# Performance work log

Measured on AMD Instinct MI355X. Metric: run time of the kernel, lower is better.

## Reference

```python
import jax, jax.numpy as jnp
import numpy as np

B, S, E, H, Dh = 2, 2048, 1024, 16, 64


def setup_inputs() -> dict:
    key = jax.random.key(0)
    ks = jax.random.split(key, 12)
    scale = 1.0 / np.sqrt(E)
    inp = {
        "query": jax.random.normal(ks[0], (B, S, E), jnp.float32),
        "key_": jax.random.normal(ks[1], (B, S, E), jnp.float32),
        "value": jax.random.normal(ks[2], (B, S, E), jnp.float32),
        # causal mask, broadcast over heads inside reference (mask==0 -> -inf)
        "mask": jnp.broadcast_to(jnp.tril(jnp.ones((S, S), jnp.int32)), (B, S, S)),
        "WQ": jax.random.normal(ks[3], (E, H * Dh), jnp.float32) * scale,
        "bQ": jnp.zeros((H * Dh,), jnp.float32),
        "WK": jax.random.normal(ks[4], (E, H * Dh), jnp.float32) * scale,
        "bK": jnp.zeros((H * Dh,), jnp.float32),
        "WV": jax.random.normal(ks[5], (E, H * Dh), jnp.float32) * scale,
        "bV": jnp.zeros((H * Dh,), jnp.float32),
        "WO": jax.random.normal(ks[6], (H * Dh, E), jnp.float32) * scale,
        "bO": jnp.zeros((E,), jnp.float32),
    }
    return inp


def reference(query, key_, value, mask, WQ, bQ, WK, bK, WV, bV, WO, bO):
    # projections -> [B, H, S, Dh]
    def proj(x, W, b):
        y = x @ W + b  # [B, S, H*Dh]
        return y.reshape(B, -1, H, Dh).transpose(0, 2, 1, 3)

    q = proj(query, WQ, bQ)
    k = proj(key_, WK, bK)
    v = proj(value, WV, bV)

    # scores [B, H, S, S]
    a = jnp.einsum("bhqd,bhkd->bhqk", q, k) / jnp.sqrt(jnp.float32(Dh))
    a = jnp.where(mask[:, None, :, :] == 0, -jnp.inf, a)
    alpha = jax.nn.softmax(a, axis=-1)
    z = jnp.einsum("bhqk,bhkd->bhqd", alpha, v)  # [B, H, S, Dh]
    z = z.transpose(0, 2, 1, 3).reshape(B, -1, H * Dh)
    return z @ WO + bO
```

## Files before the change

### kernel.cpp

```cpp
#include <hip/hip_runtime.h>
#include <hip/hip_bf16.h>
#include <math.h>

namespace {

constexpr int Bb = 2, Ss = 2048, Ee = 1024, Hh = 16, Dh = 64;
constexpr int M  = Bb * Ss;
constexpr int N  = Hh * Dh;
constexpr int Kd = Ee;

typedef __attribute__((ext_vector_type(8))) short bf16x8;
typedef __attribute__((ext_vector_type(4))) float f32x4;

__device__ inline float bflo(unsigned u) { return __uint_as_float(u << 16); }
__device__ inline float bfhi(unsigned u) { return __uint_as_float(u & 0xffff0000u); }
__device__ inline unsigned short f2bf(float f) {
  return __builtin_bit_cast(unsigned short, __float2bfloat16(f));
}
__device__ inline unsigned pack2(float a, float b) {
  return (unsigned)f2bf(a) | ((unsigned)f2bf(b) << 16);
}
__device__ inline void load_lds16(const void* g, void* lds) {
  __builtin_amdgcn_global_load_lds((const __attribute__((address_space(1))) void*)g,
                                   (__attribute__((address_space(3))) void*)lds, 16, 0, 0);
}

__global__ __launch_bounds__(256) void convert3(const float* __restrict__ a0,
                                                const float* __restrict__ a1,
                                                const float* __restrict__ a2,
                                                unsigned short* __restrict__ o0,
                                                unsigned short* __restrict__ o1,
                                                unsigned short* __restrict__ o2) {
  const float* src = blockIdx.z == 0 ? a0 : (blockIdx.z == 1 ? a1 : a2);
  unsigned short* dst = blockIdx.z == 0 ? o0 : (blockIdx.z == 1 ? o1 : o2);
  size_t i = ((size_t)blockIdx.x * 256 + threadIdx.x) * 8;
  float4 u = ((const float4*)(src + i))[0];
  float4 v = ((const float4*)(src + i))[1];
  uint4 w;
  w.x = pack2(u.x, u.y);
  w.y = pack2(u.z, u.w);
  w.z = pack2(v.x, v.y);
  w.w = pack2(v.z, v.w);
  *((uint4*)(dst + i)) = w;
}

__global__ __launch_bounds__(256) void transposeW(const float* __restrict__ w0,
                                                  const float* __restrict__ w1,
                                                  const float* __restrict__ w2,
                                                  const float* __restrict__ w3,
                                                  unsigned short* __restrict__ t0,
                                                  unsigned short* __restrict__ t1,
                                                  unsigned short* __restrict__ t2,
                                                  unsigned short* __restrict__ t3) {
  const float* W = blockIdx.z == 0 ? w0 : (blockIdx.z == 1 ? w1 : (blockIdx.z == 2 ? w2 : w3));
  unsigned short* Wt = blockIdx.z == 0 ? t0 : (blockIdx.z == 1 ? t1 : (blockIdx.z == 2 ? t2 : t3));
  __shared__ float tl[32][33];
  const int t = threadIdx.x;
  const int r = t >> 5, c = t & 31;
  const int n0 = blockIdx.x * 32, k0 = blockIdx.y * 32;
#pragma unroll
  for (int i = 0; i < 4; ++i) tl[r + i * 8][c] = W[(size_t)(k0 + r + i * 8) * N + n0 + c];
  __syncthreads();
#pragma unroll
  for (int i = 0; i < 4; ++i) {
    int rr = r + i * 8;
    Wt[(size_t)(n0 + rr) * Kd + k0 + c] = f2bf(tl[c][rr]);
  }
}

template <int PERM>
__global__ __launch_bounds__(256) void gemm_mfma(const unsigned short* __restrict__ A,
                                                 const unsigned short* __restrict__ Wt,
                                                 const float* __restrict__ bias,
                                                 void* __restrict__ Cout, float oscale) {
  __shared__ alignas(16) unsigned short As[128 * 32];
  __shared__ alignas(16) unsigned short Bs[128 * 32];

  const int t  = threadIdx.x;
  const int l  = t & 63;
  const int w  = t >> 6;
  const int wr = w >> 1, wc = w & 1;
  const int lr = l & 15, kc = l >> 4;
  const int bm = blockIdx.y * 128, bn = blockIdx.x * 128;

  f32x4 acc[4][4] = {};

  const int srow = t >> 2, sc = t & 3;
  unsigned short* aD1 = As + (size_t)(w * 64) * 8;
  unsigned short* aD2 = As + (size_t)(w * 64 + 256) * 8;
  unsigned short* bD1 = Bs + (size_t)(w * 64) * 8;
  unsigned short* bD2 = Bs + (size_t)(w * 64 + 256) * 8;
  const unsigned short* Ap1 = A  + (size_t)(bm + srow) * Kd + sc * 8;
  const unsigned short* Ap2 = A  + (size_t)(bm + srow + 64) * Kd + sc * 8;
  const unsigned short* Bp1 = Wt + (size_t)(bn + srow) * Kd + sc * 8;
  const unsigned short* Bp2 = Wt + (size_t)(bn + srow + 64) * Kd + sc * 8;

  for (int kk = 0; kk < Kd; kk += 32) {
    load_lds16(Ap1 + kk, aD1);
    load_lds16(Ap2 + kk, aD2);
    load_lds16(Bp1 + kk, bD1);
    load_lds16(Bp2 + kk, bD2);
    __syncthreads();

    bf16x8 a[4], b[4];
#pragma unroll
    for (int m = 0; m < 4; ++m)
      a[m] = *(const bf16x8*)&As[(size_t)(wr * 64 + m * 16 + lr) * 32 + kc * 8];
#pragma unroll
    for (int n = 0; n < 4; ++n)
      b[n] = *(const bf16x8*)&Bs[(size_t)(wc * 64 + n * 16 + lr) * 32 + kc * 8];
#pragma unroll
    for (int m = 0; m < 4; ++m)
#pragma unroll
      for (int n = 0; n < 4; ++n)
        acc[m][n] = __builtin_amdgcn_mfma_f32_16x16x32_bf16(a[m], b[n], acc[m][n], 0, 0, 0);
    __syncthreads();
  }

#pragma unroll
  for (int m = 0; m < 4; ++m) {
#pragma unroll
    for (int n = 0; n < 4; ++n) {
      const int cg = bn + wc * 64 + n * 16 + lr;
      const float bv = bias[cg];
      f32x4 v = acc[m][n];
      if (PERM == 2) {
        const int rg0 = bm + wr * 64 + m * 16 + kc * 4;
        const int b_ = rg0 >> 11, s0 = rg0 & (Ss - 1);
        const int h = cg >> 6, d = cg & (Dh - 1);
        ushort4 pk;
        pk.x = f2bf((v[0] + bv) * oscale);
        pk.y = f2bf((v[1] + bv) * oscale);
        pk.z = f2bf((v[2] + bv) * oscale);
        pk.w = f2bf((v[3] + bv) * oscale);
        *(ushort4*)((unsigned short*)Cout +
                    (((size_t)(b_ * Hh + h) * Dh + d) << 11) + s0) = pk;
      } else {
#pragma unroll
        for (int r = 0; r < 4; ++r) {
          const int rg  = bm + wr * 64 + m * 16 + kc * 4 + r;
          const float x = (v[r] + bv) * oscale;
          if (PERM == 0) {
            ((float*)Cout)[(size_t)rg * N + cg] = x;
          } else {
            const int b_ = rg >> 11, s = rg & (Ss - 1);
            const int h  = cg >> 6, d = cg & (Dh - 1);
            ((unsigned short*)Cout)[(((size_t)(b_ * Hh + h) * Ss + s) << 6) + d] = f2bf(x);
          }
        }
      }
    }
  }
}

__global__ __launch_bounds__(256) void attn_mfma(const unsigned short* __restrict__ Q,
                                                 const unsigned short* __restrict__ K,
                                                 const unsigned short* __restrict__ Vt,
                                                 unsigned short* __restrict__ Z) {
  __shared__ alignas(16) unsigned short Ks[64 * 64];
  __shared__ alignas(16) unsigned short Vs[64 * 64];
  __shared__ alignas(16) unsigned short Ps[4][16 * 64];

  const int bh = blockIdx.x;
  const int qt = blockIdx.y;
  const int b  = bh >> 4, h = bh & 15;
  const int t  = threadIdx.x;
  const int l  = t & 63;
  const int w  = t >> 6;
  const int lr = l & 15;
  const int lg = l >> 4;

  const int qrow = qt * 64 + w * 16 + lr;
  const unsigned short* Qp = Q + ((size_t)bh * Ss + qrow) * Dh;
  bf16x8 bq[2];
  bq[0] = *(const bf16x8*)(Qp + lg * 8);
  bq[1] = *(const bf16x8*)(Qp + 32 + lg * 8);

  f32x4 o[4] = {};
  float mrow = -INFINITY, lsum = 0.f;

  const int srow = l >> 3;
  const int scol = ((l & 7) ^ srow) * 16;
  const char* Kg = (const char*)(K + (size_t)bh * Ss * Dh);
  const char* Vg = (const char*)(Vt + (size_t)bh * Dh * Ss);
  unsigned short* kD0 = Ks + (w * 16) * 64;
  unsigned short* kD1 = Ks + (w * 16 + 8) * 64;
  unsigned short* vD0 = Vs + (w * 16) * 64;
  unsigned short* vD1 = Vs + (w * 16 + 8) * 64;
  const char* vr0 = Vg + (size_t)(w * 16 + srow) * (Ss * 2) + scol;
  const char* vr1 = Vg + (size_t)(w * 16 + 8 + srow) * (Ss * 2) + scol;

  const int rx = (lr & 7) << 4;

  const int kv_tiles = qt + 1;
  for (int kt = 0; kt < kv_tiles; ++kt) {
    const int kv0 = kt * 64;
    __syncthreads();
    load_lds16(Kg + (size_t)(kv0 + w * 16 + srow) * 128 + scol, kD0);
    load_lds16(Kg + (size_t)(kv0 + w * 16 + 8 + srow) * 128 + scol, kD1);
    load_lds16(vr0 + kv0 * 2, vD0);
    load_lds16(vr1 + kv0 * 2, vD1);
    __syncthreads();

    f32x4 sa[4];
#pragma unroll
    for (int f = 0; f < 4; ++f) {
      sa[f] = (f32x4){0.f, 0.f, 0.f, 0.f};
#pragma unroll
      for (int kk = 0; kk < 2; ++kk) {
        const int cb = (kk * 64 + lg * 16) ^ rx;
        bf16x8 ak = *(const bf16x8*)((const char*)Ks + (f * 16 + lr) * 128 + cb);
        sa[f] = __builtin_amdgcn_mfma_f32_16x16x32_bf16(ak, bq[kk], sa[f], 0, 0, 0);
      }
    }

    if (kt == kv_tiles - 1) {
#pragma unroll
      for (int f = 0; f < 4; ++f)
#pragma unroll
        for (int r = 0; r < 4; ++r) {
          const int kg = kv0 + f * 16 + lg * 4 + r;
          if (kg > qrow) sa[f][r] = -INFINITY;
        }
    }

    float pmax = sa[0][0];
#pragma unroll
    for (int f = 0; f < 4; ++f)
#pragma unroll
      for (int r = 0; r < 4; ++r) pmax = fmaxf(pmax, sa[f][r]);
    pmax = fmaxf(pmax, __shfl_xor(pmax, 16));
    pmax = fmaxf(pmax, __shfl_xor(pmax, 32));
    const float mnew = fmaxf(mrow, pmax);
    const float sc   = __expf(mrow - mnew);

    float p[4][4];
    float psum = 0.f;
#pragma unroll
    for (int f = 0; f < 4; ++f)
#pragma unroll
      for (int r = 0; r < 4; ++r) {
        p[f][r] = __expf(sa[f][r] - mnew);
        psum += p[f][r];
      }
    psum += __shfl_xor(psum, 16);
    psum += __shfl_xor(psum, 32);
    lsum = lsum * sc + psum;
    mrow = mnew;

    float scr[4];
#pragma unroll
    for (int r = 0; r < 4; ++r) scr[r] = __shfl(sc, lg * 4 + r);
#pragma unroll
    for (int n = 0; n < 4; ++n)
#pragma unroll
      for (int r = 0; r < 4; ++r) o[n][r] *= scr[r];

    {
      char* Pw = (char*)Ps[w] + lr * 128;
#pragma unroll
      for (int f = 0; f < 4; ++f) {
        const int k0b = f * 32 + lg * 8;
        *(unsigned*)(Pw + ((k0b) ^ rx))     = pack2(p[f][0], p[f][1]);
        *(unsigned*)(Pw + ((k0b + 4) ^ rx)) = pack2(p[f][2], p[f][3]);
      }
    }

#pragma unroll
    for (int kk = 0; kk < 2; ++kk) {
      const int cb = (kk * 64 + lg * 16) ^ rx;
      bf16x8 ap = *(const bf16x8*)((const char*)Ps[w] + lr * 128 + cb);
#pragma unroll
      for (int n = 0; n < 4; ++n) {
        bf16x8 bv = *(const bf16x8*)((const char*)Vs + (n * 16 + lr) * 128 + cb);
        o[n] = __builtin_amdgcn_mfma_f32_16x16x32_bf16(ap, bv, o[n], 0, 0, 0);
      }
    }
  }

  const float linv = 1.f / lsum;
  float li[4];
#pragma unroll
  for (int r = 0; r < 4; ++r) li[r] = __shfl(linv, lg * 4 + r);
#pragma unroll
  for (int n = 0; n < 4; ++n)
#pragma unroll
    for (int r = 0; r < 4; ++r) {
      const int qg = qt * 64 + w * 16 + lg * 4 + r;
      Z[((size_t)(b * Ss + qg)) * N + h * 64 + n * 16 + lr] =
          f2bf(o[n][r] * li[r]);
    }
}

}

extern "C" void kernel_launch(void* const* d_in, const int* in_sizes, int n_in,
                              void* d_out, int out_size, void* d_ws, size_t ws_size,
                              hipStream_t stream) {
  const float* query = (const float*)d_in[0];
  const float* key_  = (const float*)d_in[1];
  const float* value = (const float*)d_in[2];
  const float* WQ = (const float*)d_in[4];
  const float* bQ = (const float*)d_in[5];
  const float* WK = (const float*)d_in[6];
  const float* bK = (const float*)d_in[7];
  const float* WV = (const float*)d_in[8];
  const float* bV = (const float*)d_in[9];
  const float* WO = (const float*)d_in[10];
  const float* bO = (const float*)d_in[11];
  float* out = (float*)d_out;

  const size_t mat = (size_t)M * N;
  unsigned short* qb  = (unsigned short*)d_ws;
  unsigned short* kb  = qb + mat;
  unsigned short* vb  = kb + mat;
  unsigned short* wqT = vb + mat;
  unsigned short* wkT = wqT + (size_t)N * Kd;
  unsigned short* wvT = wkT + (size_t)N * Kd;
  unsigned short* woT = wvT + (size_t)N * Kd;
  unsigned short* Qw  = woT + (size_t)N * Kd;
  unsigned short* Kw  = Qw + mat;
  unsigned short* Vw  = Kw + mat;
  unsigned short* zb  = qb;

  convert3<<<dim3(mat / (256 * 8), 1, 3), 256, 0, stream>>>(query, key_, value, qb, kb, vb);
  transposeW<<<dim3(N / 32, Kd / 32, 4), 256, 0, stream>>>(WQ, WK, WV, WO, wqT, wkT, wvT, woT);

  dim3 gGemm(N / 128, M / 128);
  gemm_mfma<1><<<gGemm, 256, 0, stream>>>(qb, wqT, bQ, Qw, 0.125f);
  gemm_mfma<1><<<gGemm, 256, 0, stream>>>(kb, wkT, bK, Kw, 1.0f);
  gemm_mfma<2><<<gGemm, 256, 0, stream>>>(vb, wvT, bV, Vw, 1.0f);

  dim3 gAttn(Bb * Hh, Ss / 64);
  attn_mfma<<<gAttn, 256, 0, stream>>>(Qw, Kw, Vw, zb);

  gemm_mfma<0><<<gGemm, 256, 0, stream>>>(zb, woT, bO, out, 1.0f);
}
```

Measured before the change: 300.6 us.

## Double-buffer GEMM LDS tiles, batch QKV projections, stage V transpose via LDS

The GEMM main loop now uses two LDS buffers, so the async global-to-LDS load of the next K-slice is issued while MFMAs run on the current one. The three Q/K/V projection launches are merged into one grid with a z dimension, which cuts launch overhead and fills the GPU with more blocks. The transposed V output is first staged through LDS and then written with coalesced 16-byte stores instead of scattered 8-byte ones. The cost is twice the LDS per block, which may lower occupancy, plus extra barriers in the V epilogue.

```diff
diff --git a/kernel.cpp b/kernel.cpp
--- a/kernel.cpp
+++ b/kernel.cpp
@@ -12,8 +12,6 @@
 typedef __attribute__((ext_vector_type(8))) short bf16x8;
 typedef __attribute__((ext_vector_type(4))) float f32x4;
 
-__device__ inline float bflo(unsigned u) { return __uint_as_float(u << 16); }
-__device__ inline float bfhi(unsigned u) { return __uint_as_float(u & 0xffff0000u); }
 __device__ inline unsigned short f2bf(float f) {
   return __builtin_bit_cast(unsigned short, __float2bfloat16(f));
 }
@@ -68,89 +66,151 @@
   }
 }
 
-template <int PERM>
-__global__ __launch_bounds__(256) void gemm_mfma(const unsigned short* __restrict__ A,
-                                                 const unsigned short* __restrict__ Wt,
-                                                 const float* __restrict__ bias,
-                                                 void* __restrict__ Cout, float oscale) {
-  __shared__ alignas(16) unsigned short As[128 * 32];
-  __shared__ alignas(16) unsigned short Bs[128 * 32];
-
-  const int t  = threadIdx.x;
-  const int l  = t & 63;
-  const int w  = t >> 6;
-  const int wr = w >> 1, wc = w & 1;
-  const int lr = l & 15, kc = l >> 4;
+__device__ __attribute__((always_inline)) inline void gemm_core(
+    const unsigned short* __restrict__ A, const unsigned short* __restrict__ Wt,
+    unsigned short* As0, unsigned short* As1, unsigned short* Bs0,
+    unsigned short* Bs1, f32x4 (&acc)[4][4]) {
+  const int t = threadIdx.x, l = t & 63, w = t >> 6;
+  const int wr = w >> 1, wc = w & 1, lr = l & 15, kc = l >> 4;
   const int bm = blockIdx.y * 128, bn = blockIdx.x * 128;
-
-  f32x4 acc[4][4] = {};
-
-  const int srow = t >> 2, sc = t & 3;
-  unsigned short* aD1 = As + (size_t)(w * 64) * 8;
-  unsigned short* aD2 = As + (size_t)(w * 64 + 256) * 8;
-  unsigned short* bD1 = Bs + (size_t)(w * 64) * 8;
-  unsigned short* bD2 = Bs + (size_t)(w * 64 + 256) * 8;
-  const unsigned short* Ap1 = A  + (size_t)(bm + srow) * Kd + sc * 8;
-  const unsigned short* Ap2 = A  + (size_t)(bm + srow + 64) * Kd + sc * 8;
-  const unsigned short* Bp1 = Wt + (size_t)(bn + srow) * Kd + sc * 8;
-  const unsigned short* Bp2 = Wt + (size_t)(bn + srow + 64) * Kd + sc * 8;
-
-  for (int kk = 0; kk < Kd; kk += 32) {
-    load_lds16(Ap1 + kk, aD1);
-    load_lds16(Ap2 + kk, aD2);
-    load_lds16(Bp1 + kk, bD1);
-    load_lds16(Bp2 + kk, bD2);
-    __syncthreads();
-
+  const int srow = t >> 2, sc4 = t & 3;
+  const unsigned short* Ap1 = A + (size_t)(bm + srow) * Kd + sc4 * 8;
+  const unsigned short* Ap2 = Ap1 + (size_t)64 * Kd;
+  const unsigned short* Bp1 = Wt + (size_t)(bn + srow) * Kd + sc4 * 8;
+  const unsigned short* Bp2 = Bp1 + (size_t)64 * Kd;
+  const size_t d1 = (size_t)(w * 64) * 8, d2 = (size_t)(w * 64 + 256) * 8;
+
+  auto stage = [&](unsigned short* Ab, unsigned short* Bb, int kk) {
+    load_lds16(Ap1 + kk, Ab + d1);
+    load_lds16(Ap2 + kk, Ab + d2);
+    load_lds16(Bp1 + kk, Bb + d1);
+    load_lds16(Bp2 + kk, Bb + d2);
+  };
+  auto compute = [&](const unsigned short* Ab, const unsigned short* Bb) {
     bf16x8 a[4], b[4];
 #pragma unroll
     for (int m = 0; m < 4; ++m)
-      a[m] = *(const bf16x8*)&As[(size_t)(wr * 64 + m * 16 + lr) * 32 + kc * 8];
+      a[m] = *(const bf16x8*)&Ab[(size_t)(wr * 64 + m * 16 + lr) * 32 + kc * 8];
 #pragma unroll
     for (int n = 0; n < 4; ++n)
-      b[n] = *(const bf16x8*)&Bs[(size_t)(wc * 64 + n * 16 + lr) * 32 + kc * 8];
+      b[n] = *(const bf16x8*)&Bb[(size_t)(wc * 64 + n * 16 + lr) * 32 + kc * 8];
 #pragma unroll
     for (int m = 0; m < 4; ++m)
 #pragma unroll
       for (int n = 0; n < 4; ++n)
         acc[m][n] = __builtin_amdgcn_mfma_f32_16x16x32_bf16(a[m], b[n], acc[m][n], 0, 0, 0);
+  };
+
+  stage(As0, Bs0, 0);
+  __syncthreads();
+  for (int kk = 0; kk < Kd; kk += 64) {
+    if (kk + 32 < Kd) stage(As1, Bs1, kk + 32);
+    compute(As0, Bs0);
+    __syncthreads();
+    if (kk + 64 < Kd) stage(As0, Bs0, kk + 64);
+    compute(As1, Bs1);
     __syncthreads();
   }
-
-#pragma unroll
-  for (int m = 0; m < 4; ++m) {
+}
+
+__global__ __launch_bounds__(256) void qkv_gemm(
+    const unsigned short* __restrict__ qb, const unsigned short* __restrict__ kb,
+    const unsigned short* __restrict__ vb, const unsigned short* __restrict__ wqT,
+    const unsigned short* __restrict__ wkT, const unsigned short* __restrict__ wvT,
+    const float* __restrict__ bQ, const float* __restrict__ bK,
+    const float* __restrict__ bV, unsigned short* __restrict__ Qw,
+    unsigned short* __restrict__ Kw, unsigned short* __restrict__ Vt) {
+  __shared__ alignas(16) unsigned short smem[4][128 * 32];
+  const int z = blockIdx.z;
+  const unsigned short* A  = z == 0 ? qb : (z == 1 ? kb : vb);
+  const unsigned short* Wt = z == 0 ? wqT : (z == 1 ? wkT : wvT);
+  const float* bias        = z == 0 ? bQ : (z == 1 ? bK : bV);
+
+  f32x4 acc[4][4] = {};
+  gemm_core(A, Wt, smem[0], smem[1], smem[2], smem[3], acc);
+
+  const int t = threadIdx.x, l = t & 63, w = t >> 6;
+  const int wr = w >> 1, wc = w & 1, lr = l & 15, kc = l >> 4;
+  const int bm = blockIdx.y * 128, bn = blockIdx.x * 128;
+
+  if (z <= 1) {
+    unsigned short* Cout = z ? Kw : Qw;
+    const float oscale = z ? 1.0f : 0.125f;
+#pragma unroll
+    for (int m = 0; m < 4; ++m)
+#pragma unroll
+      for (int n = 0; n < 4; ++n) {
+        const int cg = bn + wc * 64 + n * 16 + lr;
+        const float bv = bias[cg];
+#pragma unroll
+        for (int r = 0; r < 4; ++r) {
+          const int rg = bm + wr * 64 + m * 16 + kc * 4 + r;
+          const int b_ = rg >> 11, s = rg & (Ss - 1);
+          const int h = cg >> 6, d = cg & 63;
+          Cout[(((size_t)(b_ * Hh + h) * Ss + s) << 6) + d] =
+              f2bf((acc[m][n][r] + bv) * oscale);
+        }
+      }
+  } else {
+    unsigned short(*Ct)[136] = reinterpret_cast<unsigned short(*)[136]>(&smem[0][0]);
+    const int b_ = bm >> 11, sb = bm & (Ss - 1);
+#pragma unroll
+    for (int nh = 0; nh < 2; ++nh) {
+      if (wc == nh) {
+#pragma unroll
+        for (int m = 0; m < 4; ++m)
+#pragma unroll
+          for (int n = 0; n < 4; ++n) {
+            const int cg = bn + wc * 64 + n * 16 + lr;
+            const float bv = bias[cg];
+            const int cl = n * 16 + lr;
+            const int s0 = wr * 64 + m * 16 + kc * 4;
+            ushort4 pk;
+            pk.x = f2bf(acc[m][n][0] + bv);
+            pk.y = f2bf(acc[m][n][1] + bv);
+            pk.z = f2bf(acc[m][n][2] + bv);
+            pk.w = f2bf(acc[m][n][3] + bv);
+            *(ushort4*)&Ct[cl][s0] = pk;
+          }
+      }
+      __syncthreads();
+#pragma unroll
+      for (int i = 0; i < 4; ++i) {
+        const int c = i * 256 + t;
+        const int cl = c >> 4, ch = c & 15;
+        const int cg = bn + nh * 64 + cl;
+        const int h = cg >> 6, d = cg & 63;
+        uint4 vv = *(const uint4*)&Ct[cl][ch * 8];
+        *(uint4*)(Vt + (((size_t)(b_ * Hh + h) * Dh + d) << 11) + sb + ch * 8) = vv;
+      }
+      __syncthreads();
+    }
+  }
+}
+
+__global__ __launch_bounds__(256) void gemm_out(const unsigned short* __restrict__ A,
+                                                const unsigned short* __restrict__ Wt,
+                                                const float* __restrict__ bias,
+                                                float* __restrict__ C) {
+  __shared__ alignas(16) unsigned short smem[4][128 * 32];
+  f32x4 acc[4][4] = {};
+  gemm_core(A, Wt, smem[0], smem[1], smem[2], smem[3], acc);
+
+  const int t = threadIdx.x, l = t & 63, w = t >> 6;
+  const int wr = w >> 1, wc = w & 1, lr = l & 15, kc = l >> 4;
+  const int bm = blockIdx.y * 128, bn = blockIdx.x * 128;
+#pragma unroll
+  for (int m = 0; m < 4; ++m)
 #pragma unroll
     for (int n = 0; n < 4; ++n) {
       const int cg = bn + wc * 64 + n * 16 + lr;
       const float bv = bias[cg];
-      f32x4 v = acc[m][n];
-      if (PERM == 2) {
-        const int rg0 = bm + wr * 64 + m * 16 + kc * 4;
-        const int b_ = rg0 >> 11, s0 = rg0 & (Ss - 1);
-        const int h = cg >> 6, d = cg & (Dh - 1);
-        ushort4 pk;
-        pk.x = f2bf((v[0] + bv) * oscale);
-        pk.y = f2bf((v[1] + bv) * oscale);
-        pk.z = f2bf((v[2] + bv) * oscale);
-        pk.w = f2bf((v[3] + bv) * oscale);
-        *(ushort4*)((unsigned short*)Cout +
-                    (((size_t)(b_ * Hh + h) * Dh + d) << 11) + s0) = pk;
-      } else {
-#pragma unroll
-        for (int r = 0; r < 4; ++r) {
-          const int rg  = bm + wr * 64 + m * 16 + kc * 4 + r;
-          const float x = (v[r] + bv) * oscale;
-          if (PERM == 0) {
-            ((float*)Cout)[(size_t)rg * N + cg] = x;
-          } else {
-            const int b_ = rg >> 11, s = rg & (Ss - 1);
-            const int h  = cg >> 6, d = cg & (Dh - 1);
-            ((unsigned short*)Cout)[(((size_t)(b_ * Hh + h) * Ss + s) << 6) + d] = f2bf(x);
-          }
-        }
-      }
-    }
-  }
+#pragma unroll
+      for (int r = 0; r < 4; ++r) {
+        const int rg = bm + wr * 64 + m * 16 + kc * 4 + r;
+        C[(size_t)rg * N + cg] = acc[m][n][r] + bv;
+      }
+    }
 }
 
 __global__ __launch_bounds__(256) void attn_mfma(const unsigned short* __restrict__ Q,
@@ -323,16 +383,13 @@
   unsigned short* Vw  = Kw + mat;
   unsigned short* zb  = qb;
 
-  convert3<<<dim3(mat / (256 * 8), 1, 3), 256, 0, stream>>>(query, key_, value, qb, kb, vb);
+  convert3<<<dim3(mat / 2048, 1, 3), 256, 0, stream>>>(query, key_, value, qb, kb, vb);
   transposeW<<<dim3(N / 32, Kd / 32, 4), 256, 0, stream>>>(WQ, WK, WV, WO, wqT, wkT, wvT, woT);
 
-  dim3 gGemm(N / 128, M / 128);
-  gemm_mfma<1><<<gGemm, 256, 0, stream>>>(qb, wqT, bQ, Qw, 0.125f);
-  gemm_mfma<1><<<gGemm, 256, 0, stream>>>(kb, wkT, bK, Kw, 1.0f);
-  gemm_mfma<2><<<gGemm, 256, 0, stream>>>(vb, wvT, bV, Vw, 1.0f);
-
-  dim3 gAttn(Bb * Hh, Ss / 64);
-  attn_mfma<<<gAttn, 256, 0, stream>>>(Qw, Kw, Vw, zb);
-
-  gemm_mfma<0><<<gGemm, 256, 0, stream>>>(zb, woT, bO, out, 1.0f);
-}
+  qkv_gemm<<<dim3(N / 128, M / 128, 3), 256, 0, stream>>>(qb, kb, vb, wqT, wkT, wvT,
+                                                          bQ, bK, bV, Qw, Kw, Vw);
+
+  attn_mfma<<<dim3(Bb * Hh, Ss / 64), 256, 0, stream>>>(Qw, Kw, Vw, zb);
+
+  gemm_out<<<dim3(N / 128, M / 128), 256, 0, stream>>>(zb, woT, bO, out);
+}
```

After: 267.5 us. 1.12x faster.
